# Kernel optimization log

Hardware: AMD Instinct MI355X
Metric: run time of the kernel (lower is better)

The kernel has to match this reference:

```python
import jax, jax.numpy as jnp
import numpy as np

B, S, H, P2 = 64, 512, 768, 46  # batch, seq, hidden, num_p*2


def setup_inputs() -> dict:
    key = jax.random.key(0)
    k1, k2, k3, k4 = jax.random.split(key, 4)
    hidden_states = jax.random.normal(k1, (B, S, H), dtype=jnp.float32)
    # subject start/end indices must lie within the valid (masked-in) prefix
    lengths = jax.random.randint(k2, (B,), S // 4, S + 1)  # cue lengths per sample
    input_mask = (jnp.arange(S)[None, :] < lengths[:, None]).astype(jnp.int32)
    ids = jax.random.randint(k3, (B, 2), 0, S // 4)
    batch_subject_ids = jnp.sort(ids, axis=1).astype(jnp.int32)
    W = jax.random.normal(k4, (P2, H), dtype=jnp.float32) * (1.0 / np.sqrt(H))
    b = jnp.zeros((P2,), dtype=jnp.float32)
    return {"hidden_states": hidden_states, "batch_subject_ids": batch_subject_ids,
            "input_mask": input_mask, "W": W, "b": b}


def reference(hidden_states, batch_subject_ids, input_mask, W, b):
    # per-sample subject embedding: h[b, start] + h[b, end]  -> [B, H]
    batch_idx = jnp.arange(hidden_states.shape[0])
    s = (hidden_states[batch_idx, batch_subject_ids[:, 0]]
         + hidden_states[batch_idx, batch_subject_ids[:, 1]])
    # broadcast-add s to the first cue_len positions of each sample
    cue_len = jnp.sum(input_mask, axis=1)  # [B]
    pos_mask = (jnp.arange(hidden_states.shape[1])[None, :] < cue_len[:, None])  # [B, S]
    h = hidden_states + s[:, None, :] * pos_mask[:, :, None].astype(hidden_states.dtype)
    # linear + sigmoid^4 (dropout is identity in eval mode)
    logits = jnp.einsum('bsh,ph->bsp', h, W) + b
    return jax.nn.sigmoid(logits) ** 4
```

## Files before the change

kernel.cpp:

```cpp
#include <hip/hip_runtime.h>
#include <hip/hip_bf16.h>

#define SEQ 512
#define HID 768
#define P2  46
#define MT  32
#define BLK 512
#define NSTEP (HID / 32)
#define QSTRIDE 48

typedef short bf16x8 __attribute__((ext_vector_type(8)));
typedef float f32x4  __attribute__((ext_vector_type(4)));

__device__ __forceinline__ unsigned short f2bf(float f) {
  union { float f; unsigned int u; } v; v.f = f;
  return (unsigned short)((v.u + 0x7FFFu + ((v.u >> 16) & 1u)) >> 16);
}

__device__ __forceinline__ unsigned short fcvt(float f) {
  __hip_bfloat16 x = __float2bfloat16(f);
  return *reinterpret_cast<unsigned short*>(&x);
}

__global__ __launch_bounds__(64) void prep_kernel(
    const float* __restrict__ h, const int* __restrict__ ids,
    const float* __restrict__ W, unsigned short* __restrict__ Wb,
    float* __restrict__ q) {
  int b = blockIdx.x, p = blockIdx.y, lane = threadIdx.x;
  const float* w = W + (size_t)p * HID;
  if (b == 0) {
    #pragma unroll
    for (int j = 0; j < HID / 64; ++j)
      Wb[p * HID + lane + j * 64] = f2bf(w[lane + j * 64]);
    if (p < 2) {
      #pragma unroll
      for (int j = 0; j < HID / 64; ++j)
        Wb[(P2 + p) * HID + lane + j * 64] = 0;
    }
  }
  int i0 = ids[b * 2 + 0], i1 = ids[b * 2 + 1];
  const float* r0 = h + ((size_t)b * SEQ + i0) * HID;
  const float* r1 = h + ((size_t)b * SEQ + i1) * HID;
  float acc = 0.f;
  #pragma unroll
  for (int j = 0; j < HID / 64; ++j) {
    int k = lane + j * 64;
    acc += (r0[k] + r1[k]) * w[k];
  }
  #pragma unroll
  for (int off = 32; off > 0; off >>= 1) acc += __shfl_down(acc, off, 64);
  if (lane == 0) q[b * QSTRIDE + p] = acc;
}

__global__ __launch_bounds__(BLK, 4) void main_kernel(
    const float* __restrict__ h, const int* __restrict__ mask,
    const unsigned short* __restrict__ Wb, const float* __restrict__ bias,
    const float* __restrict__ q, float* __restrict__ out) {
  __shared__ __align__(16) unsigned short hA[MT][HID];

  const int tid  = threadIdx.x;
  const int lane = tid & 63, wv = tid >> 6;
  const int mr = lane & 15, qd = lane >> 4;
  const int row0 = blockIdx.x * MT;
  const int b    = row0 >> 9;

  const float* hblk = h + (size_t)row0 * HID;
  #pragma unroll
  for (int i = 0; i < 12; ++i) {
    int g = i * BLK + tid;
    float4 v = *(const float4*)(hblk + ((size_t)g << 2));
    int r  = g / 192;
    int f  = g - r * 192;
    int c  = f >> 1, hc = f & 1;
    int cs = (c & 0x78) | ((c ^ r) & 7);
    ushort4 u;
    u.x = fcvt(v.x); u.y = fcvt(v.y); u.z = fcvt(v.z); u.w = fcvt(v.w);
    *(ushort4*)&hA[r][(cs << 3) + (hc << 2)] = u;
  }
  __syncthreads();

  if (wv >= 6) return;
  const int wm = wv & 1, nt = wv >> 1;

  const int rloc = (wm << 4) + mr;
  const unsigned short* wbp = Wb + (size_t)((nt << 4) + mr) * HID + (qd << 3);

  const int grow = row0 + rloc;
  const int mk   = mask[grow];
  const int p0   = (nt << 4) + (qd << 2);
  const float* qrow = q + b * QSTRIDE;
  float bv[4], qv[4];
  #pragma unroll
  for (int i = 0; i < 4; ++i) {
    bv[i] = (p0 + i < P2) ? bias[p0 + i] : 0.f;
    qv[i] = qrow[p0 + i];
  }

  f32x4 acc = f32x4{0.f, 0.f, 0.f, 0.f};
  #pragma unroll
  for (int s = 0; s < NSTEP; ++s) {
    int c  = (s << 2) + qd;
    int cs = (c & 0x78) | ((c ^ (rloc & 7)) & 7);
    bf16x8 a  = *(const bf16x8*)&hA[rloc][cs << 3];
    bf16x8 wf = *(const bf16x8*)(wbp + (s << 5));
    acc = __builtin_amdgcn_mfma_f32_16x16x32_bf16(wf, a, acc, 0, 0, 0);
  }

  float* orow = out + (size_t)grow * P2;
  float o[4];
  #pragma unroll
  for (int i = 0; i < 4; ++i) {
    float x = acc[i] + bv[i] + (mk ? qv[i] : 0.f);
    float sg = 1.f / (1.f + __expf(-x));
    sg *= sg; sg *= sg;
    o[i] = sg;
  }
  if (p0 + 1 < P2) *(float2*)(orow + p0)     = make_float2(o[0], o[1]);
  if (p0 + 3 < P2) *(float2*)(orow + p0 + 2) = make_float2(o[2], o[3]);
}

extern "C" void kernel_launch(void* const* d_in, const int* in_sizes, int n_in,
                              void* d_out, int out_size, void* d_ws, size_t ws_size,
                              hipStream_t stream) {
  const float* h    = (const float*)d_in[0];
  const int*   ids  = (const int*)d_in[1];
  const int*   mask = (const int*)d_in[2];
  const float* W    = (const float*)d_in[3];
  const float* bias = (const float*)d_in[4];
  float* out = (float*)d_out;

  unsigned short* Wb = (unsigned short*)d_ws;
  float* q = (float*)((char*)d_ws + 48 * HID * sizeof(unsigned short));

  prep_kernel<<<dim3(64, P2), 64, 0, stream>>>(h, ids, W, Wb, q);
  main_kernel<<<dim3((64 * SEQ) / MT), BLK, 0, stream>>>(h, mask, Wb, bias, q, out);
}
```

Measured before the change: 166.1 us.

## Fuse prep into main kernel, convert W on the fly, compute subject projection per block

Removes the separate prep kernel and its launch. Each block now converts fp32 W to bf16 inside the MFMA loop. The two otherwise idle waves recompute the per-batch subject projection q into shared memory while the other waves run the matmul. The global-to-LDS load indexing is also reworked so each wave loads whole rows. This drops one launch and the dependency between the two kernels, at the cost of redundant q computation in every block (1024 blocks each redoing a 46x768 dot product) and extra per-step conversion work.

Result: slower. 192.6 us (+16.0%).

```diff
diff --git a/kernel.cpp b/kernel.cpp
--- a/kernel.cpp
+++ b/kernel.cpp
@@ -7,56 +7,21 @@
 #define MT  32
 #define BLK 512
 #define NSTEP (HID / 32)
-#define QSTRIDE 48
 
 typedef short bf16x8 __attribute__((ext_vector_type(8)));
 typedef float f32x4  __attribute__((ext_vector_type(4)));
-
-__device__ __forceinline__ unsigned short f2bf(float f) {
-  union { float f; unsigned int u; } v; v.f = f;
-  return (unsigned short)((v.u + 0x7FFFu + ((v.u >> 16) & 1u)) >> 16);
-}
 
 __device__ __forceinline__ unsigned short fcvt(float f) {
   __hip_bfloat16 x = __float2bfloat16(f);
   return *reinterpret_cast<unsigned short*>(&x);
 }
 
-__global__ __launch_bounds__(64) void prep_kernel(
+__global__ __launch_bounds__(BLK, 4) void fused_kernel(
     const float* __restrict__ h, const int* __restrict__ ids,
-    const float* __restrict__ W, unsigned short* __restrict__ Wb,
-    float* __restrict__ q) {
-  int b = blockIdx.x, p = blockIdx.y, lane = threadIdx.x;
-  const float* w = W + (size_t)p * HID;
-  if (b == 0) {
-    #pragma unroll
-    for (int j = 0; j < HID / 64; ++j)
-      Wb[p * HID + lane + j * 64] = f2bf(w[lane + j * 64]);
-    if (p < 2) {
-      #pragma unroll
-      for (int j = 0; j < HID / 64; ++j)
-        Wb[(P2 + p) * HID + lane + j * 64] = 0;
-    }
-  }
-  int i0 = ids[b * 2 + 0], i1 = ids[b * 2 + 1];
-  const float* r0 = h + ((size_t)b * SEQ + i0) * HID;
-  const float* r1 = h + ((size_t)b * SEQ + i1) * HID;
-  float acc = 0.f;
-  #pragma unroll
-  for (int j = 0; j < HID / 64; ++j) {
-    int k = lane + j * 64;
-    acc += (r0[k] + r1[k]) * w[k];
-  }
-  #pragma unroll
-  for (int off = 32; off > 0; off >>= 1) acc += __shfl_down(acc, off, 64);
-  if (lane == 0) q[b * QSTRIDE + p] = acc;
-}
-
-__global__ __launch_bounds__(BLK, 4) void main_kernel(
-    const float* __restrict__ h, const int* __restrict__ mask,
-    const unsigned short* __restrict__ Wb, const float* __restrict__ bias,
-    const float* __restrict__ q, float* __restrict__ out) {
+    const int* __restrict__ mask, const float* __restrict__ W,
+    const float* __restrict__ bias, float* __restrict__ out) {
   __shared__ __align__(16) unsigned short hA[MT][HID];
+  __shared__ __align__(16) float q_s[48];
 
   const int tid  = threadIdx.x;
   const int lane = tid & 63, wv = tid >> 6;
@@ -67,10 +32,9 @@
   const float* hblk = h + (size_t)row0 * HID;
   #pragma unroll
   for (int i = 0; i < 12; ++i) {
-    int g = i * BLK + tid;
-    float4 v = *(const float4*)(hblk + ((size_t)g << 2));
-    int r  = g / 192;
-    int f  = g - r * 192;
+    const int r = (wv << 2) + (i / 3);
+    const int f = ((i % 3) << 6) + lane;
+    float4 v = *(const float4*)(hblk + ((size_t)(r * 192 + f) << 2));
     int c  = f >> 1, hc = f & 1;
     int cs = (c & 0x78) | ((c ^ r) & 7);
     ushort4 u;
@@ -79,38 +43,66 @@
   }
   __syncthreads();
 
+  f32x4 acc = f32x4{0.f, 0.f, 0.f, 0.f};
+  int nt = 0;
+
+  if (wv < 6) {
+    const int wm = wv & 1;  nt = wv >> 1;
+    const int rloc = (wm << 4) + mr;
+    int wrow = (nt << 4) + mr;
+    if (wrow > P2 - 1) wrow = P2 - 1;
+    const float* wp = W + (size_t)wrow * HID + (qd << 3);
+
+    #pragma unroll
+    for (int s = 0; s < NSTEP; ++s) {
+      int c  = (s << 2) + qd;
+      int cs = (c & 0x78) | ((c ^ (rloc & 7)) & 7);
+      bf16x8 a = *(const bf16x8*)&hA[rloc][cs << 3];
+      float4 w0 = *(const float4*)(wp + (s << 5));
+      float4 w1 = *(const float4*)(wp + (s << 5) + 4);
+      bf16x8 wf = { (short)fcvt(w0.x), (short)fcvt(w0.y),
+                    (short)fcvt(w0.z), (short)fcvt(w0.w),
+                    (short)fcvt(w1.x), (short)fcvt(w1.y),
+                    (short)fcvt(w1.z), (short)fcvt(w1.w) };
+      acc = __builtin_amdgcn_mfma_f32_16x16x32_bf16(wf, a, acc, 0, 0, 0);
+    }
+  } else {
+    const int i0 = ids[b * 2 + 0], i1 = ids[b * 2 + 1];
+    const float* r0p = h + ((size_t)b * SEQ + i0) * HID;
+    const float* r1p = h + ((size_t)b * SEQ + i1) * HID;
+    float hs[12];
+    #pragma unroll
+    for (int j = 0; j < 12; ++j) {
+      int k = lane + (j << 6);
+      hs[j] = r0p[k] + r1p[k];
+    }
+    if (wv == 6 && lane == 0) { q_s[46] = 0.f; q_s[47] = 0.f; }
+    const int pbase = (wv - 6) * 23;
+    for (int j = 0; j < 23; ++j) {
+      const float* wrow = W + (size_t)(pbase + j) * HID;
+      float a = 0.f;
+      #pragma unroll
+      for (int k = 0; k < 12; ++k)
+        a += hs[k] * wrow[lane + (k << 6)];
+      #pragma unroll
+      for (int off = 32; off > 0; off >>= 1) a += __shfl_xor(a, off, 64);
+      if (lane == 0) q_s[pbase + j] = a;
+    }
+  }
+  __syncthreads();
   if (wv >= 6) return;
-  const int wm = wv & 1, nt = wv >> 1;
 
-  const int rloc = (wm << 4) + mr;
-  const unsigned short* wbp = Wb + (size_t)((nt << 4) + mr) * HID + (qd << 3);
-
+  const int rloc = ((wv & 1) << 4) + mr;
   const int grow = row0 + rloc;
   const int mk   = mask[grow];
   const int p0   = (nt << 4) + (qd << 2);
-  const float* qrow = q + b * QSTRIDE;
-  float bv[4], qv[4];
-  #pragma unroll
-  for (int i = 0; i < 4; ++i) {
-    bv[i] = (p0 + i < P2) ? bias[p0 + i] : 0.f;
-    qv[i] = qrow[p0 + i];
-  }
-
-  f32x4 acc = f32x4{0.f, 0.f, 0.f, 0.f};
-  #pragma unroll
-  for (int s = 0; s < NSTEP; ++s) {
-    int c  = (s << 2) + qd;
-    int cs = (c & 0x78) | ((c ^ (rloc & 7)) & 7);
-    bf16x8 a  = *(const bf16x8*)&hA[rloc][cs << 3];
-    bf16x8 wf = *(const bf16x8*)(wbp + (s << 5));
-    acc = __builtin_amdgcn_mfma_f32_16x16x32_bf16(wf, a, acc, 0, 0, 0);
-  }
-
+  float4 qv = *(const float4*)&q_s[p0];
   float* orow = out + (size_t)grow * P2;
   float o[4];
   #pragma unroll
   for (int i = 0; i < 4; ++i) {
-    float x = acc[i] + bv[i] + (mk ? qv[i] : 0.f);
+    float bv = (p0 + i < P2) ? bias[p0 + i] : 0.f;
+    float x = acc[i] + bv + (mk ? ((const float*)&qv)[i] : 0.f);
     float sg = 1.f / (1.f + __expf(-x));
     sg *= sg; sg *= sg;
     o[i] = sg;
@@ -129,9 +121,5 @@
   const float* bias = (const float*)d_in[4];
   float* out = (float*)d_out;
 
-  unsigned short* Wb = (unsigned short*)d_ws;
-  float* q = (float*)((char*)d_ws + 48 * HID * sizeof(unsigned short));
-
-  prep_kernel<<<dim3(64, P2), 64, 0, stream>>>(h, ids, W, Wb, q);
-  main_kernel<<<dim3((64 * SEQ) / MT), BLK, 0, stream>>>(h, mask, Wb, bias, q, out);
+  fused_kernel<<<dim3((64 * SEQ) / MT), BLK, 0, stream>>>(h, ids, mask, W, bias, out);
 }
```

## Stage fp32 rows via async global-to-LDS loads and preload weights into registers

Applied to the files above, without the earlier changes.

The hidden-state tile is now copied straight from global memory into LDS as fp32 with direct global_load_lds instructions, using a swizzled source address in place of a register round-trip that converted to bf16. Conversion to bf16 moves into the MFMA loop, reading fp32 from LDS. The tile shrinks to 16 rows with 256 threads, and each compute wave preloads all its bf16 weight fragments into registers while the async copy is in flight. The cost is double the LDS per row, more LDS read traffic and conversion work inside the inner loop, a 24-register weight array per thread, and one of four waves sitting idle after the load.

New measurement: 164.5 us. About the same (-1.0%).

```diff
diff --git a/kernel.cpp b/kernel.cpp
--- a/kernel.cpp
+++ b/kernel.cpp
@@ -4,8 +4,8 @@
 #define SEQ 512
 #define HID 768
 #define P2  46
-#define MT  32
-#define BLK 512
+#define MT  16
+#define BLK 256
 #define NSTEP (HID / 32)
 #define QSTRIDE 48
 
@@ -20,6 +20,12 @@
 __device__ __forceinline__ unsigned short fcvt(float f) {
   __hip_bfloat16 x = __float2bfloat16(f);
   return *reinterpret_cast<unsigned short*>(&x);
+}
+
+__device__ __forceinline__ void async_ld16(const void* g, void* l) {
+  __builtin_amdgcn_global_load_lds(
+      (const __attribute__((address_space(1))) unsigned int*)g,
+      (__attribute__((address_space(3))) unsigned int*)l, 16, 0, 0);
 }
 
 __global__ __launch_bounds__(64) void prep_kernel(
@@ -52,11 +58,11 @@
   if (lane == 0) q[b * QSTRIDE + p] = acc;
 }
 
-__global__ __launch_bounds__(BLK, 4) void main_kernel(
+__global__ __launch_bounds__(BLK, 3) void main_kernel(
     const float* __restrict__ h, const int* __restrict__ mask,
     const unsigned short* __restrict__ Wb, const float* __restrict__ bias,
     const float* __restrict__ q, float* __restrict__ out) {
-  __shared__ __align__(16) unsigned short hA[MT][HID];
+  __shared__ __align__(16) float hA[MT][HID];
 
   const int tid  = threadIdx.x;
   const int lane = tid & 63, wv = tid >> 6;
@@ -66,44 +72,52 @@
 
   const float* hblk = h + (size_t)row0 * HID;
   #pragma unroll
-  for (int i = 0; i < 12; ++i) {
-    int g = i * BLK + tid;
-    float4 v = *(const float4*)(hblk + ((size_t)g << 2));
-    int r  = g / 192;
-    int f  = g - r * 192;
-    int c  = f >> 1, hc = f & 1;
-    int cs = (c & 0x78) | ((c ^ r) & 7);
-    ushort4 u;
-    u.x = fcvt(v.x); u.y = fcvt(v.y); u.z = fcvt(v.z); u.w = fcvt(v.w);
-    *(ushort4*)&hA[r][(cs << 3) + (hc << 2)] = u;
-  }
-  __syncthreads();
-
-  if (wv >= 6) return;
-  const int wm = wv & 1, nt = wv >> 1;
-
-  const int rloc = (wm << 4) + mr;
-  const unsigned short* wbp = Wb + (size_t)((nt << 4) + mr) * HID + (qd << 3);
-
-  const int grow = row0 + rloc;
-  const int mk   = mask[grow];
-  const int p0   = (nt << 4) + (qd << 2);
-  const float* qrow = q + b * QSTRIDE;
-  float bv[4], qv[4];
-  #pragma unroll
-  for (int i = 0; i < 4; ++i) {
-    bv[i] = (p0 + i < P2) ? bias[p0 + i] : 0.f;
-    qv[i] = qrow[p0 + i];
+  for (int j = 0; j < 12; ++j) {
+    const int r   = (wv << 2) + j / 3;
+    const int seg = j % 3;
+    int c  = (seg << 6) + lane;
+    int gg = c >> 1;
+    int gs = (gg & ~7) | ((gg ^ r) & 7);
+    const float* src = hblk + (size_t)r * HID + ((gs << 1) | (c & 1)) * 4;
+    async_ld16(src, &hA[r][seg << 8]);
   }
 
+  const int nt = wv;
+  bf16x8 wf[NSTEP];
   f32x4 acc = f32x4{0.f, 0.f, 0.f, 0.f};
+  int mk = 0, p0 = 0, grow = 0;
+  float bv[4], qv[4];
+  if (wv < 3) {
+    const unsigned short* wbp = Wb + (size_t)((nt << 4) + mr) * HID + (qd << 3);
+    #pragma unroll
+    for (int s = 0; s < NSTEP; ++s)
+      wf[s] = *(const bf16x8*)(wbp + (s << 5));
+    grow = row0 + mr;
+    mk   = mask[grow];
+    p0   = (nt << 4) + (qd << 2);
+    const float* qrow = q + b * QSTRIDE;
+    #pragma unroll
+    for (int i = 0; i < 4; ++i) {
+      bv[i] = (p0 + i < P2) ? bias[p0 + i] : 0.f;
+      qv[i] = qrow[p0 + i];
+    }
+  }
+
+  __syncthreads();
+  if (wv >= 3) return;
+
   #pragma unroll
   for (int s = 0; s < NSTEP; ++s) {
-    int c  = (s << 2) + qd;
-    int cs = (c & 0x78) | ((c ^ (rloc & 7)) & 7);
-    bf16x8 a  = *(const bf16x8*)&hA[rloc][cs << 3];
-    bf16x8 wf = *(const bf16x8*)(wbp + (s << 5));
-    acc = __builtin_amdgcn_mfma_f32_16x16x32_bf16(wf, a, acc, 0, 0, 0);
+    int gg = (s << 2) + qd;
+    int gs = (gg & ~7) | ((gg ^ mr) & 7);
+    const float* fp = &hA[mr][gs << 3];
+    float4 a0 = *(const float4*)fp;
+    float4 a1 = *(const float4*)(fp + 4);
+    bf16x8 hb = { (short)fcvt(a0.x), (short)fcvt(a0.y),
+                  (short)fcvt(a0.z), (short)fcvt(a0.w),
+                  (short)fcvt(a1.x), (short)fcvt(a1.y),
+                  (short)fcvt(a1.z), (short)fcvt(a1.w) };
+    acc = __builtin_amdgcn_mfma_f32_16x16x32_bf16(wf[s], hb, acc, 0, 0, 0);
   }
 
   float* orow = out + (size_t)grow * P2;
```
